# Optimization experiments

Hardware: AMD Instinct MI355X
Metric: run time of the kernel (lower is better)

Reference implementation:

```python
import jax, jax.numpy as jnp
import numpy as np

N_NODES, N_EDGES, H = 50000, 800000, 96


def setup_inputs() -> dict:
    key = jax.random.key(0)
    ks = jax.random.split(key, 8)
    s = 1.0 / np.sqrt(H)  # xavier-ish scale
    g = lambda k, shape, sc=1.0: jax.random.normal(k, shape, jnp.float32) * sc
    return {
        "x": g(ks[0], (N_NODES, H)),
        "conn": g(ks[1], (N_EDGES, H)),
        "edge_index": jax.random.randint(ks[2], (2, N_EDGES), 0, N_NODES),  # row0=dst, row1=src
        "qkv_w": g(ks[3], (3 * H, H), s),
        "qkv_b": jnp.zeros((3 * H,), jnp.float32),
        "e_w": g(ks[4], (2 * H, H), s),
        "e_b": jnp.zeros((2 * H,), jnp.float32),
        "conn_lin_w": g(ks[5], (H, H), s),
        "conn_lin_b": jnp.zeros((H,), jnp.float32),
        "nodelin_w": g(ks[6], (H, H), s),
        "nodelin_b": jnp.zeros((H,), jnp.float32),
        "ln_h_g": jnp.ones((H,), jnp.float32),
        "ln_h_b": jnp.zeros((H,), jnp.float32),
        "ln_e_g": jnp.ones((H,), jnp.float32),
        "ln_e_b": jnp.zeros((H,), jnp.float32),
    }


def _layernorm(v, g, b, eps=1e-5):
    mu = v.mean(-1, keepdims=True)
    var = ((v - mu) ** 2).mean(-1, keepdims=True)
    return (v - mu) * jax.lax.rsqrt(var + eps) * g + b


def reference(x, conn, edge_index, qkv_w, qkv_b, e_w, e_b, conn_lin_w, conn_lin_b,
              nodelin_w, nodelin_b, ln_h_g, ln_h_b, ln_e_g, ln_e_b):
    n = x.shape[0]
    # packed QKV projection (attn_dim*attn_heads == hidden_dim)
    qkv = x @ qkv_w.T + qkv_b                      # [N, 3H]
    Qh, Kh, Vh = jnp.split(qkv, 3, axis=-1)        # each [N, H]
    # edge feature projection -> (Ew, Eb)
    Eh = (conn @ e_w.T + e_b).reshape(conn.shape[0], 2, H)  # [E, 2, H]
    Ew, Eb = Eh[:, 0, :], Eh[:, 1, :]
    dst, src = edge_index[0], edge_index[1]
    # gather -> elementwise signed-sqrt -> activation
    c1 = (Qh[dst] + Kh[src]) * Ew                  # [E, H]
    c2 = jnp.sign(c1) * jnp.sqrt(jnp.abs(c1))      # == sqrt(relu(c1)) - sqrt(relu(-c1))
    conn_out = jax.nn.relu(c2 + Eb)                # [E, H]
    # scatter-reduce (agg='add')
    agg = jax.ops.segment_sum(Vh[src], dst, num_segments=n)            # [N, H]
    eagg = jax.ops.segment_sum(conn_out, dst, num_segments=n)          # [N, H]
    eagg = eagg @ conn_lin_w.T + conn_lin_b
    h = (agg + eagg) @ nodelin_w.T + nodelin_b     # nodelin (dropout p=0)
    h = x + h                                      # residual
    e = conn + conn_out
    return _layernorm(h, ln_h_g, ln_h_b), _layernorm(e, ln_e_g, ln_e_b)
```

## Files before the change

kernel.cpp:

```cpp
#include <hip/hip_runtime.h>
#include <math.h>

#define N_NODES 50000
#define N_EDGES 800000
#define H 96
#define QKV_N 288

#define NPB1 32
#define NPB3 4

typedef __attribute__((ext_vector_type(8))) short short8;
typedef __attribute__((ext_vector_type(4))) float f32x4;

__device__ __forceinline__ short f2bf(float f) {
    union { float f; unsigned u; } v; v.f = f;
    unsigned r = v.u + 0x7FFFu + ((v.u >> 16) & 1u);
    return (short)(r >> 16);
}
__device__ __forceinline__ float bf2f(unsigned short h) {
    union { unsigned u; float f; } v; v.u = ((unsigned)h) << 16;
    return v.f;
}

__device__ __forceinline__ void ld_frag_split(const float* __restrict__ p,
                                              short8& hi, short8& lo) {
    float4 a = *(const float4*)p;
    float4 b = *(const float4*)(p + 4);
    float f[8] = {a.x, a.y, a.z, a.w, b.x, b.y, b.z, b.w};
    #pragma unroll
    for (int j = 0; j < 8; ++j) {
        short h = f2bf(f[j]);
        hi[j] = h;
        lo[j] = f2bf(f[j] - bf2f((unsigned short)h));
    }
}

__global__ __launch_bounds__(QKV_N) void qkv_kernel(
    const float* __restrict__ x, const float* __restrict__ qw,
    const float* __restrict__ qb, float* __restrict__ qkv)
{
    __shared__ __align__(16) float xs[H];
    const int t = threadIdx.x;

    float w[H];
    #pragma unroll
    for (int k4 = 0; k4 < H; k4 += 4) {
        float4 v = *(const float4*)(qw + (size_t)t * H + k4);
        w[k4] = v.x; w[k4 + 1] = v.y; w[k4 + 2] = v.z; w[k4 + 3] = v.w;
    }
    const float bias = qb[t];

    const int n0 = blockIdx.x * NPB1;
    for (int nn = 0; nn < NPB1; ++nn) {
        const int node = n0 + nn;
        if (node >= N_NODES) break;
        __syncthreads();
        if (t < H) xs[t] = x[(size_t)node * H + t];
        __syncthreads();
        float acc = bias;
        #pragma unroll
        for (int k4 = 0; k4 < H; k4 += 4) {
            float4 c = *(const float4*)(xs + k4);
            acc += c.x * w[k4] + c.y * w[k4 + 1] + c.z * w[k4 + 2] + c.w * w[k4 + 3];
        }
        qkv[(size_t)node * QKV_N + t] = acc;
    }
}

__global__ __launch_bounds__(256) void hist_kernel(const int* __restrict__ eidx,
                                                   int* __restrict__ hist) {
    const int e = blockIdx.x * 256 + threadIdx.x;
    if (e < N_EDGES) atomicAdd(&hist[eidx[e]], 1);
}

#define SCAN_CH 49
__global__ __launch_bounds__(1024) void scan_kernel(int* __restrict__ hist,
                                                    int* __restrict__ rowptr) {
    __shared__ int sums[1024];
    const int t = threadIdx.x;
    const int st = t * SCAN_CH;
    int loc = 0;
    for (int k = 0; k < SCAN_CH; ++k) {
        const int i = st + k;
        if (i < N_NODES) loc += hist[i];
    }
    sums[t] = loc;
    __syncthreads();
    for (int off = 1; off < 1024; off <<= 1) {
        int add = (t >= off) ? sums[t - off] : 0;
        __syncthreads();
        sums[t] += add;
        __syncthreads();
    }
    int run = sums[t] - loc;
    for (int k = 0; k < SCAN_CH; ++k) {
        const int i = st + k;
        if (i < N_NODES) {
            const int v = hist[i];
            rowptr[i] = run;
            hist[i]   = run;
            run += v;
        }
    }
    if (t == 1023) rowptr[N_NODES] = run;
}

__global__ __launch_bounds__(256) void scatter_kernel(const int* __restrict__ eidx,
                                                      int* __restrict__ cursor,
                                                      int* __restrict__ bucket,
                                                      int* __restrict__ bsrc) {
    const int e = blockIdx.x * 256 + threadIdx.x;
    if (e < N_EDGES) {
        const int dst = eidx[e];
        const int src = eidx[N_EDGES + e];
        const int pos = atomicAdd(&cursor[dst], 1);
        bucket[pos] = e;
        bsrc[pos]   = src;
    }
}

#define TILE_E 64
#define EH_LD 196

__global__ __launch_bounds__(256) void edge_kernel(
    const float* __restrict__ conn, const int* __restrict__ eidx,
    const float* __restrict__ qkv,
    const float* __restrict__ ew, const float* __restrict__ eb,
    float* __restrict__ out_e)
{
    __shared__ float eh[TILE_E * EH_LD];

    const int t    = threadIdx.x;
    const int wave = t >> 6;
    const int lane = t & 63;
    const int lr   = lane & 15;
    const int lg16 = lane >> 4;

    short8 bwh[3][3], bwl[3][3];
    #pragma unroll
    for (int f = 0; f < 3; ++f) {
        const int tcol = 16 * (3 * wave + f) + lr;
        #pragma unroll
        for (int kc = 0; kc < 3; ++kc)
            ld_frag_split(ew + (size_t)tcol * H + 32 * kc + 8 * lg16,
                          bwh[f][kc], bwl[f][kc]);
    }

    const int e0 = blockIdx.x * TILE_E;

    f32x4 acc[4][3];
    #pragma unroll
    for (int mt = 0; mt < 4; ++mt)
        #pragma unroll
        for (int f = 0; f < 3; ++f)
            acc[mt][f] = (f32x4){0.f, 0.f, 0.f, 0.f};

    #pragma unroll
    for (int mt = 0; mt < 4; ++mt) {
        const int erow = e0 + 16 * mt + lr;
        short8 ah[3], al[3];
        #pragma unroll
        for (int kc = 0; kc < 3; ++kc)
            ld_frag_split(conn + (size_t)erow * H + 32 * kc + 8 * lg16,
                          ah[kc], al[kc]);
        #pragma unroll
        for (int f = 0; f < 3; ++f) {
            #pragma unroll
            for (int kc = 0; kc < 3; ++kc) {
                acc[mt][f] = __builtin_amdgcn_mfma_f32_16x16x32_bf16(
                                 ah[kc], bwl[f][kc], acc[mt][f], 0, 0, 0);
                acc[mt][f] = __builtin_amdgcn_mfma_f32_16x16x32_bf16(
                                 al[kc], bwh[f][kc], acc[mt][f], 0, 0, 0);
                acc[mt][f] = __builtin_amdgcn_mfma_f32_16x16x32_bf16(
                                 ah[kc], bwh[f][kc], acc[mt][f], 0, 0, 0);
            }
        }
    }

    #pragma unroll
    for (int mt = 0; mt < 4; ++mt) {
        #pragma unroll
        for (int f = 0; f < 3; ++f) {
            const int col = 16 * (3 * wave + f) + lr;
            const float bias = eb[col];
            #pragma unroll
            for (int r = 0; r < 4; ++r) {
                const int row = 16 * mt + 4 * lg16 + r;
                eh[row * EH_LD + col] = acc[mt][f][r] + bias;
            }
        }
    }
    __syncthreads();

    const int e_loc = t >> 2;
    const int q4    = t & 3;
    const int e     = e0 + e_loc;
    const int dst   = eidx[e];
    const int src   = eidx[N_EDGES + e];
    const float4* qQ4 = (const float4*)(qkv + (size_t)dst * QKV_N) + 6 * q4;
    const float4* qK4 = (const float4*)(qkv + (size_t)src * QKV_N + H) + 6 * q4;
    float4*       oe4 = (float4*)(out_e + (size_t)e * H) + 6 * q4;
    const float*  ehr = &eh[e_loc * EH_LD + 24 * q4];

    #pragma unroll
    for (int i = 0; i < 6; ++i) {
        const float4 q  = qQ4[i];
        const float4 k  = qK4[i];
        const float4 w4 = *(const float4*)(ehr + 4 * i);
        const float4 b4 = *(const float4*)(ehr + 4 * i + H);
        float4 co4;
        #pragma unroll
        for (int jj = 0; jj < 4; ++jj) {
            const float c1 = (q[jj] + k[jj]) * w4[jj];
            const float c2 = copysignf(sqrtf(fabsf(c1)), c1);
            co4[jj] = fmaxf(c2 + b4[jj], 0.f);
        }
        oe4[i] = co4;
    }
}

__global__ __launch_bounds__(256) void eln_kernel(
    const float* __restrict__ conn,
    const float* __restrict__ ln_g, const float* __restrict__ ln_b,
    float* __restrict__ out_e)
{
    const int tt   = blockIdx.x * 256 + threadIdx.x;
    const size_t e = (size_t)(tt >> 2);
    const int q4   = tt & 3;
    const float4* cn4 = (const float4*)(conn + e * H) + 6 * q4;
    float4*       oe4 = (float4*)(out_e + e * H) + 6 * q4;
    const float4* g4  = (const float4*)ln_g + 6 * q4;
    const float4* b4  = (const float4*)ln_b + 6 * q4;

    float4 v[6];
    float s = 0.f, s2 = 0.f;
    #pragma unroll
    for (int i = 0; i < 6; ++i) {
        const float4 c = cn4[i];
        const float4 o = oe4[i];
        float4 val;
        #pragma unroll
        for (int jj = 0; jj < 4; ++jj) {
            val[jj] = c[jj] + o[jj];
            s += val[jj]; s2 += val[jj] * val[jj];
        }
        v[i] = val;
    }
    s  += __shfl_xor(s, 1);  s  += __shfl_xor(s, 2);
    s2 += __shfl_xor(s2, 1); s2 += __shfl_xor(s2, 2);
    const float mean = s * (1.f / H);
    const float var  = s2 * (1.f / H) - mean * mean;
    const float rs   = rsqrtf(var + 1e-5f);
    #pragma unroll
    for (int i = 0; i < 6; ++i) {
        const float4 g = g4[i], b = b4[i];
        float4 o;
        #pragma unroll
        for (int jj = 0; jj < 4; ++jj)
            o[jj] = (v[i][jj] - mean) * rs * g[jj] + b[jj];
        oe4[i] = o;
    }
}

__global__ __launch_bounds__(192) void node_kernel(
    const float* __restrict__ x, const float* __restrict__ qkv,
    const float* __restrict__ co_f32,
    const int* __restrict__ rowptr, const int* __restrict__ bucket,
    const int* __restrict__ bsrc,
    const float* __restrict__ clw, const float* __restrict__ clb,
    const float* __restrict__ nlw, const float* __restrict__ nlb,
    const float* __restrict__ ln_g, const float* __restrict__ ln_b,
    float* __restrict__ out_h)
{
    __shared__ __align__(16) float ga[H];
    __shared__ __align__(16) float sa[H];
    __shared__ float pa2[192], pe2[192];
    __shared__ float red0[H], red1[H];
    const int t = threadIdx.x;
    const int col = (t < H) ? t : (t - H);
    const int par = (t < H) ? 0 : 1;

    float w[H];
    {
        const float* wsrc = (t < H) ? (clw + (size_t)t * H) : (nlw + (size_t)(t - H) * H);
        #pragma unroll
        for (int k4 = 0; k4 < H; k4 += 4) {
            float4 v = *(const float4*)(wsrc + k4);
            w[k4] = v.x; w[k4 + 1] = v.y; w[k4 + 2] = v.z; w[k4 + 3] = v.w;
        }
    }
    const float bias = (t < H) ? clb[t] : nlb[t - H];
    const float lg = (t >= H) ? ln_g[t - H] : 0.f;
    const float lb = (t >= H) ? ln_b[t - H] : 0.f;

    const int n0 = blockIdx.x * NPB3;
    for (int nn = 0; nn < NPB3; ++nn) {
        const int node = n0 + nn;
        if (node >= N_NODES) break;
        const int r0 = rowptr[node], r1 = rowptr[node + 1];

        float pa = 0.f, pe = 0.f;
        for (int j = r0 + par; j < r1; j += 2) {
            const int ee = bucket[j];
            const int sv = bsrc[j];
            pa += qkv[(size_t)sv * QKV_N + 2 * H + col];
            pe += co_f32[(size_t)ee * H + col];
        }
        __syncthreads();
        pa2[t] = pa; pe2[t] = pe;
        __syncthreads();
        if (t < H) ga[t]      = pe2[t] + pe2[t + H];
        else       sa[t - H]  = pa2[t - H] + pa2[t];
        __syncthreads();

        if (t < H) {
            float acc = bias;
            #pragma unroll
            for (int k4 = 0; k4 < H; k4 += 4) {
                float4 c = *(const float4*)(ga + k4);
                acc += c.x * w[k4] + c.y * w[k4 + 1] + c.z * w[k4 + 2] + c.w * w[k4 + 3];
            }
            sa[t] += acc;
        }
        __syncthreads();

        float val = 0.f;
        if (t >= H) {
            const int tt = t - H;
            float acc = bias;
            #pragma unroll
            for (int k4 = 0; k4 < H; k4 += 4) {
                float4 c = *(const float4*)(sa + k4);
                acc += c.x * w[k4] + c.y * w[k4 + 1] + c.z * w[k4 + 2] + c.w * w[k4 + 3];
            }
            val = acc + x[(size_t)node * H + tt];
            red0[tt] = val;
            red1[tt] = val * val;
        }
        __syncthreads();
        if (t < 32) { red0[t] += red0[t + 64]; red1[t] += red1[t + 64]; }
        __syncthreads();
        for (int s = 32; s > 0; s >>= 1) {
            if (t < s) { red0[t] += red0[t + s]; red1[t] += red1[t + s]; }
            __syncthreads();
        }
        if (t >= H) {
            const float mean = red0[0] * (1.f / H);
            const float var  = red1[0] * (1.f / H) - mean * mean;
            const float r    = rsqrtf(var + 1e-5f);
            out_h[(size_t)node * H + (t - H)] = (val - mean) * r * lg + lb;
        }
    }
}

extern "C" void kernel_launch(void* const* d_in, const int* in_sizes, int n_in,
                              void* d_out, int out_size, void* d_ws, size_t ws_size,
                              hipStream_t stream) {
    const float* x      = (const float*)d_in[0];
    const float* conn   = (const float*)d_in[1];
    const int*   eidx   = (const int*)  d_in[2];
    const float* qkv_w  = (const float*)d_in[3];
    const float* qkv_b  = (const float*)d_in[4];
    const float* e_w    = (const float*)d_in[5];
    const float* e_b    = (const float*)d_in[6];
    const float* clw    = (const float*)d_in[7];
    const float* clb    = (const float*)d_in[8];
    const float* nlw    = (const float*)d_in[9];
    const float* nlb    = (const float*)d_in[10];
    const float* ln_h_g = (const float*)d_in[11];
    const float* ln_h_b = (const float*)d_in[12];
    const float* ln_e_g = (const float*)d_in[13];
    const float* ln_e_b = (const float*)d_in[14];

    float* out_h = (float*)d_out;
    float* out_e = out_h + (size_t)N_NODES * H;

    char* base = (char*)d_ws;
    float* qkv = (float*)base;
    size_t off = (size_t)N_NODES * QKV_N * sizeof(float);
    int* rowptr = (int*)(base + off); off += (size_t)(N_NODES + 1) * 4;
    int* hist   = (int*)(base + off); off += (size_t)N_NODES * 4;
    int* bucket = (int*)(base + off); off += (size_t)N_EDGES * 4;
    int* bsrc   = (int*)(base + off);

    hipMemsetAsync(hist, 0, (size_t)N_NODES * 4, stream);

    qkv_kernel    <<<(N_NODES + NPB1 - 1) / NPB1, QKV_N, 0, stream>>>(x, qkv_w, qkv_b, qkv);
    hist_kernel   <<<(N_EDGES + 255) / 256, 256, 0, stream>>>(eidx, hist);
    scan_kernel   <<<1, 1024, 0, stream>>>(hist, rowptr);
    scatter_kernel<<<(N_EDGES + 255) / 256, 256, 0, stream>>>(eidx, hist, bucket, bsrc);

    edge_kernel<<<N_EDGES / TILE_E, 256, 0, stream>>>(conn, eidx, qkv, e_w, e_b, out_e);
    node_kernel<<<(N_NODES + NPB3 - 1) / NPB3, 192, 0, stream>>>(
        x, qkv, out_e, rowptr, bucket, bsrc,
        clw, clb, nlw, nlb, ln_h_g, ln_h_b, out_h);
    eln_kernel<<<(N_EDGES * 4) / 256, 256, 0, stream>>>(conn, ln_e_g, ln_e_b, out_e);
}
```

Baseline: 1.490 ms.

## Split node stage into balanced segmented aggregation and separate node transform

Adds an aggregation kernel that splits each 32-node block's CSR edge range evenly across quads of threads. Each quad accumulates V and conn_out rows per destination node and flushes them with shared-memory atomics, so work is balanced regardless of node degree. A separate node kernel keeps the conn_lin and nodelin weights in registers and processes 8 nodes per block, doing the matmuls and layernorm from the precomputed aggregates. This costs an extra dst array, the agg/eagg intermediate buffers, and one more launch, and it only runs if the workspace is large enough.

Measured after the change: 1.726 ms. 15.8% more time.

```diff
diff --git a/kernel.cpp b/kernel.cpp
--- a/kernel.cpp
+++ b/kernel.cpp
@@ -8,6 +8,8 @@
 
 #define NPB1 32
 #define NPB3 4
+#define NPB3B 8
+#define NPA 32
 
 typedef __attribute__((ext_vector_type(8))) short short8;
 typedef __attribute__((ext_vector_type(4))) float f32x4;
@@ -108,7 +110,8 @@
 __global__ __launch_bounds__(256) void scatter_kernel(const int* __restrict__ eidx,
                                                       int* __restrict__ cursor,
                                                       int* __restrict__ bucket,
-                                                      int* __restrict__ bsrc) {
+                                                      int* __restrict__ bsrc,
+                                                      int* __restrict__ dstof) {
     const int e = blockIdx.x * 256 + threadIdx.x;
     if (e < N_EDGES) {
         const int dst = eidx[e];
@@ -116,6 +119,7 @@
         const int pos = atomicAdd(&cursor[dst], 1);
         bucket[pos] = e;
         bsrc[pos]   = src;
+        if (dstof) dstof[pos] = dst;
     }
 }
 
@@ -259,6 +263,158 @@
         for (int jj = 0; jj < 4; ++jj)
             o[jj] = (v[i][jj] - mean) * rs * g[jj] + b[jj];
         oe4[i] = o;
+    }
+}
+
+__global__ __launch_bounds__(256) void agg_kernel(
+    const float* __restrict__ qkv, const float* __restrict__ co,
+    const int* __restrict__ rowptr, const int* __restrict__ bucket,
+    const int* __restrict__ bsrc, const int* __restrict__ dstof,
+    float* __restrict__ agg, float* __restrict__ eagg)
+{
+    __shared__ float accA[NPA][H];
+    __shared__ float accE[NPA][H];
+    const int t = threadIdx.x;
+
+    for (int i = t; i < NPA * H; i += 256) {
+        ((float*)accA)[i] = 0.f;
+        ((float*)accE)[i] = 0.f;
+    }
+    __syncthreads();
+
+    const int n0   = blockIdx.x * NPA;
+    const int nend = (n0 + NPA < N_NODES) ? (n0 + NPA) : N_NODES;
+    const int P0 = rowptr[n0], P1 = rowptr[nend];
+    const int count = P1 - P0;
+    const int quad = t >> 2, q4 = t & 3;
+    const int len  = (count + 63) >> 6;
+    int p    = P0 + quad * len;
+    int pend = p + len; if (pend > P1) pend = P1;
+
+    float4 va[6], ve[6];
+    #pragma unroll
+    for (int i = 0; i < 6; ++i) { va[i] = (float4){0,0,0,0}; ve[i] = (float4){0,0,0,0}; }
+    int cur = -1;
+
+    for (; p < pend; ++p) {
+        const int slot = dstof[p] - n0;
+        if (slot != cur) {
+            if (cur >= 0) {
+                #pragma unroll
+                for (int i = 0; i < 6; ++i)
+                    #pragma unroll
+                    for (int jj = 0; jj < 4; ++jj) {
+                        atomicAdd(&accA[cur][24 * q4 + 4 * i + jj], va[i][jj]);
+                        atomicAdd(&accE[cur][24 * q4 + 4 * i + jj], ve[i][jj]);
+                    }
+                #pragma unroll
+                for (int i = 0; i < 6; ++i) { va[i] = (float4){0,0,0,0}; ve[i] = (float4){0,0,0,0}; }
+            }
+            cur = slot;
+        }
+        const int e  = bucket[p];
+        const int sv = bsrc[p];
+        const float4* v4 = (const float4*)(qkv + (size_t)sv * QKV_N + 2 * H) + 6 * q4;
+        const float4* c4 = (const float4*)(co + (size_t)e * H) + 6 * q4;
+        #pragma unroll
+        for (int i = 0; i < 6; ++i) {
+            const float4 a = v4[i];
+            const float4 b = c4[i];
+            #pragma unroll
+            for (int jj = 0; jj < 4; ++jj) { va[i][jj] += a[jj]; ve[i][jj] += b[jj]; }
+        }
+    }
+    if (cur >= 0) {
+        #pragma unroll
+        for (int i = 0; i < 6; ++i)
+            #pragma unroll
+            for (int jj = 0; jj < 4; ++jj) {
+                atomicAdd(&accA[cur][24 * q4 + 4 * i + jj], va[i][jj]);
+                atomicAdd(&accE[cur][24 * q4 + 4 * i + jj], ve[i][jj]);
+            }
+    }
+    __syncthreads();
+
+    const int nloc = nend - n0;
+    for (int i = t; i < nloc * H; i += 256) {
+        const int r = i / H, c = i - r * H;
+        agg [(size_t)(n0 + r) * H + c] = accA[r][c];
+        eagg[(size_t)(n0 + r) * H + c] = accE[r][c];
+    }
+}
+
+__global__ __launch_bounds__(192) void node_kernel_big(
+    const float* __restrict__ x,
+    const float* __restrict__ agg, const float* __restrict__ eagg,
+    const float* __restrict__ clw, const float* __restrict__ clb,
+    const float* __restrict__ nlw, const float* __restrict__ nlb,
+    const float* __restrict__ ln_g, const float* __restrict__ ln_b,
+    float* __restrict__ out_h)
+{
+    __shared__ __align__(16) float ga[H];
+    __shared__ __align__(16) float sa[H];
+    __shared__ float red0[H], red1[H];
+    const int t = threadIdx.x;
+
+    float w[H];
+    {
+        const float* wsrc = (t < H) ? (clw + (size_t)t * H) : (nlw + (size_t)(t - H) * H);
+        #pragma unroll
+        for (int k4 = 0; k4 < H; k4 += 4) {
+            float4 v = *(const float4*)(wsrc + k4);
+            w[k4] = v.x; w[k4 + 1] = v.y; w[k4 + 2] = v.z; w[k4 + 3] = v.w;
+        }
+    }
+    const float bias = (t < H) ? clb[t] : nlb[t - H];
+    const float lg = (t >= H) ? ln_g[t - H] : 0.f;
+    const float lb = (t >= H) ? ln_b[t - H] : 0.f;
+
+    const int n0 = blockIdx.x * NPB3B;
+    for (int nn = 0; nn < NPB3B; ++nn) {
+        const int node = n0 + nn;
+        if (node >= N_NODES) break;
+        __syncthreads();
+        if (t < H)       ga[t]     = eagg[(size_t)node * H + t];
+        else             sa[t - H] = agg[(size_t)node * H + (t - H)];
+        __syncthreads();
+
+        if (t < H) {
+            float acc = bias;
+            #pragma unroll
+            for (int k4 = 0; k4 < H; k4 += 4) {
+                float4 c = *(const float4*)(ga + k4);
+                acc += c.x * w[k4] + c.y * w[k4 + 1] + c.z * w[k4 + 2] + c.w * w[k4 + 3];
+            }
+            sa[t] += acc;
+        }
+        __syncthreads();
+
+        float val = 0.f;
+        if (t >= H) {
+            const int tt = t - H;
+            float acc = bias;
+            #pragma unroll
+            for (int k4 = 0; k4 < H; k4 += 4) {
+                float4 c = *(const float4*)(sa + k4);
+                acc += c.x * w[k4] + c.y * w[k4 + 1] + c.z * w[k4 + 2] + c.w * w[k4 + 3];
+            }
+            val = acc + x[(size_t)node * H + tt];
+            red0[tt] = val;
+            red1[tt] = val * val;
+        }
+        __syncthreads();
+        if (t < 32) { red0[t] += red0[t + 64]; red1[t] += red1[t + 64]; }
+        __syncthreads();
+        for (int s = 32; s > 0; s >>= 1) {
+            if (t < s) { red0[t] += red0[t + s]; red1[t] += red1[t + s]; }
+            __syncthreads();
+        }
+        if (t >= H) {
+            const float mean = red0[0] * (1.f / H);
+            const float var  = red1[0] * (1.f / H) - mean * mean;
+            const float r    = rsqrtf(var + 1e-5f);
+            out_h[(size_t)node * H + (t - H)] = (val - mean) * r * lg + lb;
+        }
     }
 }
 
@@ -381,18 +537,31 @@
     int* rowptr = (int*)(base + off); off += (size_t)(N_NODES + 1) * 4;
     int* hist   = (int*)(base + off); off += (size_t)N_NODES * 4;
     int* bucket = (int*)(base + off); off += (size_t)N_EDGES * 4;
-    int* bsrc   = (int*)(base + off);
+    int* bsrc   = (int*)(base + off); off += (size_t)N_EDGES * 4;
+    int*   dstof = (int*)(base + off);  off += (size_t)N_EDGES * 4;
+    float* agg   = (float*)(base + off); off += (size_t)N_NODES * H * 4;
+    float* eagg  = (float*)(base + off); off += (size_t)N_NODES * H * 4;
+    const bool big = ws_size >= off;
 
     hipMemsetAsync(hist, 0, (size_t)N_NODES * 4, stream);
 
     qkv_kernel    <<<(N_NODES + NPB1 - 1) / NPB1, QKV_N, 0, stream>>>(x, qkv_w, qkv_b, qkv);
     hist_kernel   <<<(N_EDGES + 255) / 256, 256, 0, stream>>>(eidx, hist);
     scan_kernel   <<<1, 1024, 0, stream>>>(hist, rowptr);
-    scatter_kernel<<<(N_EDGES + 255) / 256, 256, 0, stream>>>(eidx, hist, bucket, bsrc);
+    scatter_kernel<<<(N_EDGES + 255) / 256, 256, 0, stream>>>(eidx, hist, bucket, bsrc,
+                                                              big ? dstof : nullptr);
 
     edge_kernel<<<N_EDGES / TILE_E, 256, 0, stream>>>(conn, eidx, qkv, e_w, e_b, out_e);
-    node_kernel<<<(N_NODES + NPB3 - 1) / NPB3, 192, 0, stream>>>(
-        x, qkv, out_e, rowptr, bucket, bsrc,
-        clw, clb, nlw, nlb, ln_h_g, ln_h_b, out_h);
+
+    if (big) {
+        agg_kernel<<<(N_NODES + NPA - 1) / NPA, 256, 0, stream>>>(
+            qkv, out_e, rowptr, bucket, bsrc, dstof, agg, eagg);
+        node_kernel_big<<<(N_NODES + NPB3B - 1) / NPB3B, 192, 0, stream>>>(
+            x, agg, eagg, clw, clb, nlw, nlb, ln_h_g, ln_h_b, out_h);
+    } else {
+        node_kernel<<<(N_NODES + NPB3 - 1) / NPB3, 192, 0, stream>>>(
+            x, qkv, out_e, rowptr, bucket, bsrc,
+            clw, clb, nlw, nlb, ln_h_g, ln_h_b, out_h);
+    }
     eln_kernel<<<(N_EDGES * 4) / 256, 256, 0, stream>>>(conn, ln_e_g, ln_e_b, out_e);
 }
```
